# Performance work log

Hardware: AMD Instinct MI355X
Metric: run time of the kernel (lower is better)

## Reference

```python
import jax, jax.numpy as jnp
import numpy as np

N_NODES = 50000
N_EDGES = 800000
IN_CH, HID_CH, OUT_CH = 256, 128, 64


def setup_inputs() -> dict:
    key = jax.random.key(0)
    k_x, k_e, k_w1, k_w2 = jax.random.split(key, 4)
    x = jax.random.normal(k_x, (N_NODES, IN_CH), dtype=jnp.float32)
    edge_index = jax.random.randint(k_e, (2, N_EDGES), 0, N_NODES, dtype=jnp.int32)
    # Glorot-style init like PyG GCNConv (weight [in, out], bias zeros)
    s1 = float(np.sqrt(6.0 / (IN_CH + HID_CH)))
    s2 = float(np.sqrt(6.0 / (HID_CH + OUT_CH)))
    W1 = jax.random.uniform(k_w1, (IN_CH, HID_CH), jnp.float32, -s1, s1)
    b1 = jnp.zeros((HID_CH,), jnp.float32)
    W2 = jax.random.uniform(k_w2, (HID_CH, OUT_CH), jnp.float32, -s2, s2)
    b2 = jnp.zeros((OUT_CH,), jnp.float32)
    return {"x": x, "edge_index": edge_index, "W1": W1, "b1": b1, "W2": W2, "b2": b2}


def _gcn_conv(x, src, dst, deg_inv_sqrt, W, b, n_nodes):
    """GCNConv with self-loops: D^{-1/2}(A+I)D^{-1/2} X W + b."""
    h = x @ W  # [N, out]
    norm = deg_inv_sqrt[src] * deg_inv_sqrt[dst]          # [E]
    msgs = h[src] * norm[:, None]                          # [E, out] gather
    agg = jax.ops.segment_sum(msgs, dst, num_segments=n_nodes)  # scatter-add
    self_loop = h * (deg_inv_sqrt * deg_inv_sqrt)[:, None]      # self-loop term
    return agg + self_loop + b


def reference(x, edge_index, W1, b1, W2, b2):
    n = x.shape[0]
    src, dst = edge_index[0], edge_index[1]
    # degree includes self-loop (+1), edge weight 1, counted at destination
    deg = jnp.zeros((n,), x.dtype).at[dst].add(1.0) + 1.0
    dis = jax.lax.rsqrt(deg)
    h = jax.nn.relu(_gcn_conv(x, src, dst, dis, W1, b1, n))
    out = jax.nn.relu(_gcn_conv(h, src, dst, dis, W2, b2, n))
    return out
```

## Files before the change

kernel.cpp:

```cpp
#include <hip/hip_runtime.h>

#define N_NODES 50000
#define N_EDGES 800000
#define IN_CH 256
#define HID_CH 128
#define OUT_CH 64
#define CAP 64
#define NBINS 196
#define BINCAP 8192
#define PCHUNK 3200
#define PBLOCKS 250
#define SWZ_ELEMS (IN_CH * HID_CH + HID_CH * OUT_CH)
#define SWZ_BLOCKS (SWZ_ELEMS / 256)

typedef _Float16 f16;
typedef _Float16 f16x8 __attribute__((ext_vector_type(8)));
typedef float f32x4 __attribute__((ext_vector_type(4)));
typedef unsigned short u16;
typedef unsigned int u32;

template <int K, int N>
__device__ __forceinline__ void swz(const float* __restrict__ W, f16* __restrict__ Bsw,
                                    int idx) {
    constexpr int NTILES = N / 16;
    int j = idx & 7;
    int lane = (idx >> 3) & 63;
    int rest = idx >> 9;
    int nt = rest % NTILES;
    int ks = rest / NTILES;
    int k = ks * 32 + (lane >> 4) * 8 + j;
    int n = nt * 16 + (lane & 15);
    Bsw[idx] = (f16)W[(size_t)k * N + n];
}

__global__ __launch_bounds__(256) void k_place(const int* __restrict__ src,
                                               const int* __restrict__ dst,
                                               int* __restrict__ binCursor,
                                               u32* __restrict__ ebuf,
                                               const float* __restrict__ W1,
                                               const float* __restrict__ W2,
                                               f16* __restrict__ B1,
                                               f16* __restrict__ B2) {
    if ((int)blockIdx.x >= PBLOCKS) {
        int idx = ((int)blockIdx.x - PBLOCKS) * 256 + threadIdx.x;
        if (idx < IN_CH * HID_CH) {
            swz<IN_CH, HID_CH>(W1, B1, idx);
        } else {
            idx -= IN_CH * HID_CH;
            if (idx < HID_CH * OUT_CH) swz<HID_CH, OUT_CH>(W2, B2, idx);
        }
        return;
    }
    __shared__ u32 codes[PCHUNK];
    __shared__ int lcnt[NBINS], lbase[NBINS], lcur[NBINS];
    for (int i = threadIdx.x; i < NBINS; i += 256) lcnt[i] = 0;
    __syncthreads();
    int base = blockIdx.x * PCHUNK;
    for (int j = threadIdx.x; j < PCHUNK; j += 256) {
        u32 d = (u32)dst[base + j];
        codes[j] = (d << 16) | (u32)src[base + j];
        atomicAdd(&lcnt[d >> 8], 1);
    }
    __syncthreads();
    for (int i = threadIdx.x; i < NBINS; i += 256) {
        lbase[i] = i * BINCAP + atomicAdd(&binCursor[i], lcnt[i]);
        lcur[i] = 0;
    }
    __syncthreads();
    for (int j = threadIdx.x; j < PCHUNK; j += 256) {
        u32 c = codes[j];
        int b = c >> 24;
        int p = atomicAdd(&lcur[b], 1);
        int pos = lbase[b] + p;
        if (pos < (b + 1) * BINCAP) ebuf[pos] = c;
    }
}

__global__ __launch_bounds__(256) void k_build(const u32* __restrict__ ebuf,
                                               const int* __restrict__ binCursor,
                                               int* __restrict__ cnt,
                                               float* __restrict__ dis,
                                               u16* __restrict__ bucket, int N) {
    __shared__ int lcnt[256];
    __shared__ u16 lbuck[256 * CAP];
    int t = threadIdx.x;
    lcnt[t] = 0;
    __syncthreads();
    int b = blockIdx.x;
    int count = binCursor[b];
    if (count > BINCAP) count = BINCAP;
    int s = b * BINCAP;
    int e = s + count;
    for (int i = s + t; i < e; i += 256) {
        u32 c = ebuf[i];
        int local = (c >> 16) & 255;
        int p = atomicAdd(&lcnt[local], 1);
        if (p < CAP) lbuck[local * CAP + p] = (u16)(c & 0xFFFFu);
    }
    __syncthreads();
    int nodeBase = b << 8;
    if (nodeBase + t < N) {
        cnt[nodeBase + t] = lcnt[t];
        dis[nodeBase + t] = rsqrtf((float)lcnt[t] + 1.0f);
    }
    const uint4* lsrc = (const uint4*)lbuck;
    uint4* gdst = (uint4*)(bucket + (size_t)nodeBase * CAP);
    for (int idx = t; idx < 256 * CAP / 8; idx += 256) {
        int row = idx >> 3;
        int chunk = idx & 7;
        if (nodeBase + row < N && (chunk << 3) < lcnt[row]) gdst[idx] = lsrc[idx];
    }
}

__global__ __launch_bounds__(256) void k_gemm1(const float* __restrict__ A,
                                               const f16* __restrict__ Bsw,
                                               const float* __restrict__ dis,
                                               f16* __restrict__ C, int M) {
    constexpr int K = IN_CH, N = HID_CH;
    constexpr int KSTEPS = K / 32, NTILES = N / 16;
    const int tid = threadIdx.x;
    const int wave = tid >> 6, lane = tid & 63;
    const int quad = lane >> 4, l16 = lane & 15;
    int row = blockIdx.x * 64 + wave * 16 + l16;
    const int rowc = row < M ? row : M - 1;

    f32x4 acc[NTILES];
#pragma unroll
    for (int t = 0; t < NTILES; ++t) acc[t] = (f32x4){0.f, 0.f, 0.f, 0.f};

#pragma unroll
    for (int ks = 0; ks < KSTEPS; ++ks) {
        f16x8 afrag;
        const float4* p = (const float4*)(A + (size_t)rowc * K + ks * 32 + quad * 8);
        float4 v0 = p[0], v1 = p[1];
        afrag[0] = (f16)v0.x; afrag[1] = (f16)v0.y;
        afrag[2] = (f16)v0.z; afrag[3] = (f16)v0.w;
        afrag[4] = (f16)v1.x; afrag[5] = (f16)v1.y;
        afrag[6] = (f16)v1.z; afrag[7] = (f16)v1.w;
#pragma unroll
        for (int t = 0; t < NTILES; ++t) {
            f16x8 bfrag = *(const f16x8*)(Bsw + (((size_t)ks * NTILES + t) * 64 + lane) * 8);
            acc[t] = __builtin_amdgcn_mfma_f32_16x16x32_f16(afrag, bfrag, acc[t], 0, 0, 0);
        }
    }

    int rbase = blockIdx.x * 64 + wave * 16 + quad * 4;
#pragma unroll
    for (int r = 0; r < 4; ++r) {
        int gr = rbase + r;
        if (gr < M) {
            float d = dis[gr];
#pragma unroll
            for (int t = 0; t < NTILES; ++t)
                C[(size_t)gr * N + t * 16 + l16] = (f16)(acc[t][r] * d);
        }
    }
}

__global__ __launch_bounds__(256) void k_pullgemm(const f16* __restrict__ g1,
                                                  const float* __restrict__ dis,
                                                  const float* __restrict__ b1,
                                                  const int* __restrict__ cnt,
                                                  const u16* __restrict__ bucket,
                                                  const f16* __restrict__ B2sw,
                                                  f16* __restrict__ g2) {
    constexpr int LDSW = HID_CH + 8;
    __shared__ f16 aggl[64 * LDSW];
    const int tid = threadIdx.x;
    const int sub = tid & 15;
    const int nl = tid >> 4;
    const int blockBase = (int)blockIdx.x * 64;

    const float4* b1p = (const float4*)(b1 + sub * 8);
    float4 bb0 = b1p[0], bb1 = b1p[1];
    float bv[8] = {bb0.x, bb0.y, bb0.z, bb0.w, bb1.x, bb1.y, bb1.z, bb1.w};

    for (int it = 0; it < 4; ++it) {
        int lrow = it * 16 + nl;
        int u = blockBase + lrow;
        f16x8 o;
        if (u < N_NODES) {
            const f16* gp = g1 + sub * 8;
            f16x8 sv = *(const f16x8*)(gp + (size_t)u * HID_CH);
            float a[8];
#pragma unroll
            for (int j = 0; j < 8; ++j) a[j] = (float)sv[j];

            int n = cnt[u];
            if (n > CAP) n = CAP;
            const u16* row = bucket + u * CAP;

            int k = 0;
            for (; k + 8 <= n; k += 8) {
                uint4 iv = *(const uint4*)(row + k);
                int s0 = iv.x & 0xFFFF, s1 = iv.x >> 16;
                int s2 = iv.y & 0xFFFF, s3 = iv.y >> 16;
                int s4 = iv.z & 0xFFFF, s5 = iv.z >> 16;
                int s6 = iv.w & 0xFFFF, s7 = iv.w >> 16;
                f16x8 v0 = *(const f16x8*)(gp + (size_t)s0 * HID_CH);
                f16x8 v1 = *(const f16x8*)(gp + (size_t)s1 * HID_CH);
                f16x8 v2 = *(const f16x8*)(gp + (size_t)s2 * HID_CH);
                f16x8 v3 = *(const f16x8*)(gp + (size_t)s3 * HID_CH);
                f16x8 v4 = *(const f16x8*)(gp + (size_t)s4 * HID_CH);
                f16x8 v5 = *(const f16x8*)(gp + (size_t)s5 * HID_CH);
                f16x8 v6 = *(const f16x8*)(gp + (size_t)s6 * HID_CH);
                f16x8 v7 = *(const f16x8*)(gp + (size_t)s7 * HID_CH);
#pragma unroll
                for (int j = 0; j < 8; ++j)
                    a[j] += (((float)v0[j] + (float)v1[j]) + ((float)v2[j] + (float)v3[j])) +
                            (((float)v4[j] + (float)v5[j]) + ((float)v6[j] + (float)v7[j]));
            }
            if (k + 4 <= n) {
                ushort4 s4v = *(const ushort4*)(row + k);
                f16x8 v0 = *(const f16x8*)(gp + (size_t)s4v.x * HID_CH);
                f16x8 v1 = *(const f16x8*)(gp + (size_t)s4v.y * HID_CH);
                f16x8 v2 = *(const f16x8*)(gp + (size_t)s4v.z * HID_CH);
                f16x8 v3 = *(const f16x8*)(gp + (size_t)s4v.w * HID_CH);
#pragma unroll
                for (int j = 0; j < 8; ++j)
                    a[j] += ((float)v0[j] + (float)v1[j]) + ((float)v2[j] + (float)v3[j]);
                k += 4;
            }
            for (; k < n; ++k) {
                f16x8 v = *(const f16x8*)(gp + (size_t)row[k] * HID_CH);
#pragma unroll
                for (int j = 0; j < 8; ++j) a[j] += (float)v[j];
            }

            float du = dis[u];
#pragma unroll
            for (int j = 0; j < 8; ++j) {
                float t = fmaf(du, a[j], bv[j]);
                o[j] = (f16)(t > 0.f ? t : 0.f);
            }
        } else {
#pragma unroll
            for (int j = 0; j < 8; ++j) o[j] = (f16)0;
        }
        *(f16x8*)(aggl + (size_t)lrow * LDSW + sub * 8) = o;
    }
    __syncthreads();

    constexpr int KSTEPS = HID_CH / 32, NTILES = OUT_CH / 16;
    const int wave = tid >> 6, lane = tid & 63;
    const int quad = lane >> 4, l16 = lane & 15;
    const int lrowA = wave * 16 + l16;

    f32x4 acc[NTILES];
#pragma unroll
    for (int t = 0; t < NTILES; ++t) acc[t] = (f32x4){0.f, 0.f, 0.f, 0.f};

#pragma unroll
    for (int ks = 0; ks < KSTEPS; ++ks) {
        f16x8 afrag = *(const f16x8*)(aggl + (size_t)lrowA * LDSW + ks * 32 + quad * 8);
#pragma unroll
        for (int t = 0; t < NTILES; ++t) {
            f16x8 bfrag = *(const f16x8*)(B2sw + (((size_t)ks * NTILES + t) * 64 + lane) * 8);
            acc[t] = __builtin_amdgcn_mfma_f32_16x16x32_f16(afrag, bfrag, acc[t], 0, 0, 0);
        }
    }

    int rbase = blockBase + wave * 16 + quad * 4;
#pragma unroll
    for (int r = 0; r < 4; ++r) {
        int gr = rbase + r;
        if (gr < N_NODES) {
            float d = dis[gr];
#pragma unroll
            for (int t = 0; t < NTILES; ++t)
                g2[(size_t)gr * OUT_CH + t * 16 + l16] = (f16)(acc[t][r] * d);
        }
    }
}

__global__ __launch_bounds__(256) void k_pull2(const f16* __restrict__ g2,
                                               const float* __restrict__ dis,
                                               const float* __restrict__ b2,
                                               const int* __restrict__ cnt,
                                               const u16* __restrict__ bucket,
                                               float* __restrict__ out) {
    int gtid = blockIdx.x * 256 + threadIdx.x;
    int u = gtid >> 3;
    int sub = gtid & 7;
    if (u >= N_NODES) return;
    const f16* gp = g2 + sub * 8;

    f16x8 sv = *(const f16x8*)(gp + (size_t)u * OUT_CH);
    float a[8];
#pragma unroll
    for (int j = 0; j < 8; ++j) a[j] = (float)sv[j];

    int n = cnt[u];
    if (n > CAP) n = CAP;
    const u16* row = bucket + u * CAP;

    int k = 0;
    for (; k + 8 <= n; k += 8) {
        uint4 iv = *(const uint4*)(row + k);
        int s0 = iv.x & 0xFFFF, s1 = iv.x >> 16;
        int s2 = iv.y & 0xFFFF, s3 = iv.y >> 16;
        int s4 = iv.z & 0xFFFF, s5 = iv.z >> 16;
        int s6 = iv.w & 0xFFFF, s7 = iv.w >> 16;
        f16x8 v0 = *(const f16x8*)(gp + (size_t)s0 * OUT_CH);
        f16x8 v1 = *(const f16x8*)(gp + (size_t)s1 * OUT_CH);
        f16x8 v2 = *(const f16x8*)(gp + (size_t)s2 * OUT_CH);
        f16x8 v3 = *(const f16x8*)(gp + (size_t)s3 * OUT_CH);
        f16x8 v4 = *(const f16x8*)(gp + (size_t)s4 * OUT_CH);
        f16x8 v5 = *(const f16x8*)(gp + (size_t)s5 * OUT_CH);
        f16x8 v6 = *(const f16x8*)(gp + (size_t)s6 * OUT_CH);
        f16x8 v7 = *(const f16x8*)(gp + (size_t)s7 * OUT_CH);
#pragma unroll
        for (int j = 0; j < 8; ++j)
            a[j] += (((float)v0[j] + (float)v1[j]) + ((float)v2[j] + (float)v3[j])) +
                    (((float)v4[j] + (float)v5[j]) + ((float)v6[j] + (float)v7[j]));
    }
    if (k + 4 <= n) {
        ushort4 s4v = *(const ushort4*)(row + k);
        f16x8 v0 = *(const f16x8*)(gp + (size_t)s4v.x * OUT_CH);
        f16x8 v1 = *(const f16x8*)(gp + (size_t)s4v.y * OUT_CH);
        f16x8 v2 = *(const f16x8*)(gp + (size_t)s4v.z * OUT_CH);
        f16x8 v3 = *(const f16x8*)(gp + (size_t)s4v.w * OUT_CH);
#pragma unroll
        for (int j = 0; j < 8; ++j)
            a[j] += ((float)v0[j] + (float)v1[j]) + ((float)v2[j] + (float)v3[j]);
        k += 4;
    }
    for (; k < n; ++k) {
        f16x8 v = *(const f16x8*)(gp + (size_t)row[k] * OUT_CH);
#pragma unroll
        for (int j = 0; j < 8; ++j) a[j] += (float)v[j];
    }

    float du = dis[u];
    float4* op = (float4*)(out + (size_t)u * OUT_CH + sub * 8);
    float4 o0, o1;
    o0.x = fmaxf(fmaf(du, a[0], b2[sub * 8 + 0]), 0.f);
    o0.y = fmaxf(fmaf(du, a[1], b2[sub * 8 + 1]), 0.f);
    o0.z = fmaxf(fmaf(du, a[2], b2[sub * 8 + 2]), 0.f);
    o0.w = fmaxf(fmaf(du, a[3], b2[sub * 8 + 3]), 0.f);
    o1.x = fmaxf(fmaf(du, a[4], b2[sub * 8 + 4]), 0.f);
    o1.y = fmaxf(fmaf(du, a[5], b2[sub * 8 + 5]), 0.f);
    o1.z = fmaxf(fmaf(du, a[6], b2[sub * 8 + 6]), 0.f);
    o1.w = fmaxf(fmaf(du, a[7], b2[sub * 8 + 7]), 0.f);
    op[0] = o0;
    op[1] = o1;
}


extern "C" void kernel_launch(void* const* d_in, const int* in_sizes, int n_in,
                              void* d_out, int out_size, void* d_ws, size_t ws_size,
                              hipStream_t stream) {
    const float* x  = (const float*)d_in[0];
    const int* ei   = (const int*)d_in[1];
    const float* W1 = (const float*)d_in[2];
    const float* b1 = (const float*)d_in[3];
    const float* W2 = (const float*)d_in[4];
    const float* b2 = (const float*)d_in[5];
    float* out = (float*)d_out;

    const int* src = ei;
    const int* dst = ei + N_EDGES;

    char* ws = (char*)d_ws;
    size_t off = 0;
    auto alloc = [&](size_t bytes) -> void* {
        off = (off + 255) & ~(size_t)255;
        void* p = ws + off;
        off += bytes;
        return p;
    };
    int*   binCursor = (int*)alloc((size_t)NBINS * 4);
    u32*   ebuf      = (u32*)alloc((size_t)NBINS * BINCAP * 4);
    int*   cnt       = (int*)alloc((size_t)N_NODES * 4);
    float* dis       = (float*)alloc((size_t)N_NODES * 4);
    u16*   bucket    = (u16*)alloc((size_t)N_NODES * CAP * 2);
    f16*   W1sw      = (f16*)alloc((size_t)IN_CH * HID_CH * 2);
    f16*   W2sw      = (f16*)alloc((size_t)HID_CH * OUT_CH * 2);
    f16*   g1        = (f16*)alloc((size_t)N_NODES * HID_CH * 2);
    f16*   g2        = (f16*)alloc((size_t)N_NODES * OUT_CH * 2);

    hipMemsetAsync(binCursor, 0, (size_t)NBINS * 4, stream);

    k_place<<<PBLOCKS + SWZ_BLOCKS, 256, 0, stream>>>(src, dst, binCursor, ebuf,
                                                      W1, W2, W1sw, W2sw);
    k_build<<<NBINS, 256, 0, stream>>>(ebuf, binCursor, cnt, dis, bucket, N_NODES);

    k_gemm1<<<(N_NODES + 63) / 64, 256, 0, stream>>>(x, W1sw, dis, g1, N_NODES);

    k_pullgemm<<<(N_NODES + 63) / 64, 256, 0, stream>>>(g1, dis, b1, cnt, bucket,
                                                        W2sw, g2);

    k_pull2<<<(N_NODES * 8 + 255) / 256, 256, 0, stream>>>(g2, dis, b2, cnt, bucket, out);
}
```

Baseline: 186.6 us.

## Merge bucket build and first GEMM into one launch, move source scaling to pull

The CSR bucket build and the first dense GEMM now run as a single kernel: the first NBINS blocks build the buckets and the rest compute x@W1. Because the GEMM no longer waits for degrees, it writes unscaled h. The pull kernel applies the source-side dis[s] scaling per neighbour instead. This removes a launch and the serialization between the two independent stages. In exchange each gathered edge needs an extra random 4-byte dis load and a multiply, and the large smem footprint of the build path also limits occupancy for the GEMM blocks.

```diff
diff --git a/kernel.cpp b/kernel.cpp
--- a/kernel.cpp
+++ b/kernel.cpp
@@ -12,6 +12,7 @@
 #define PBLOCKS 250
 #define SWZ_ELEMS (IN_CH * HID_CH + HID_CH * OUT_CH)
 #define SWZ_BLOCKS (SWZ_ELEMS / 256)
+#define GEMM1_BLOCKS ((N_NODES + 63) / 64)
 
 typedef _Float16 f16;
 typedef _Float16 f16x8 __attribute__((ext_vector_type(8)));
@@ -76,57 +77,57 @@
     }
 }
 
-__global__ __launch_bounds__(256) void k_build(const u32* __restrict__ ebuf,
-                                               const int* __restrict__ binCursor,
-                                               int* __restrict__ cnt,
-                                               float* __restrict__ dis,
-                                               u16* __restrict__ bucket, int N) {
+__global__ __launch_bounds__(256) void k_buildmm(const u32* __restrict__ ebuf,
+                                                 const int* __restrict__ binCursor,
+                                                 int* __restrict__ cnt,
+                                                 float* __restrict__ dis,
+                                                 u16* __restrict__ bucket,
+                                                 const float* __restrict__ A,
+                                                 const f16* __restrict__ Bsw,
+                                                 f16* __restrict__ C) {
     __shared__ int lcnt[256];
     __shared__ u16 lbuck[256 * CAP];
     int t = threadIdx.x;
-    lcnt[t] = 0;
-    __syncthreads();
-    int b = blockIdx.x;
-    int count = binCursor[b];
-    if (count > BINCAP) count = BINCAP;
-    int s = b * BINCAP;
-    int e = s + count;
-    for (int i = s + t; i < e; i += 256) {
-        u32 c = ebuf[i];
-        int local = (c >> 16) & 255;
-        int p = atomicAdd(&lcnt[local], 1);
-        if (p < CAP) lbuck[local * CAP + p] = (u16)(c & 0xFFFFu);
-    }
-    __syncthreads();
-    int nodeBase = b << 8;
-    if (nodeBase + t < N) {
-        cnt[nodeBase + t] = lcnt[t];
-        dis[nodeBase + t] = rsqrtf((float)lcnt[t] + 1.0f);
-    }
-    const uint4* lsrc = (const uint4*)lbuck;
-    uint4* gdst = (uint4*)(bucket + (size_t)nodeBase * CAP);
-    for (int idx = t; idx < 256 * CAP / 8; idx += 256) {
-        int row = idx >> 3;
-        int chunk = idx & 7;
-        if (nodeBase + row < N && (chunk << 3) < lcnt[row]) gdst[idx] = lsrc[idx];
-    }
-}
-
-__global__ __launch_bounds__(256) void k_gemm1(const float* __restrict__ A,
-                                               const f16* __restrict__ Bsw,
-                                               const float* __restrict__ dis,
-                                               f16* __restrict__ C, int M) {
+    if ((int)blockIdx.x < NBINS) {
+        lcnt[t] = 0;
+        __syncthreads();
+        int b = blockIdx.x;
+        int count = binCursor[b];
+        if (count > BINCAP) count = BINCAP;
+        int s = b * BINCAP;
+        int e = s + count;
+        for (int i = s + t; i < e; i += 256) {
+            u32 c = ebuf[i];
+            int local = (c >> 16) & 255;
+            int p = atomicAdd(&lcnt[local], 1);
+            if (p < CAP) lbuck[local * CAP + p] = (u16)(c & 0xFFFFu);
+        }
+        __syncthreads();
+        int nodeBase = b << 8;
+        if (nodeBase + t < N_NODES) {
+            cnt[nodeBase + t] = lcnt[t];
+            dis[nodeBase + t] = rsqrtf((float)lcnt[t] + 1.0f);
+        }
+        const uint4* lsrc = (const uint4*)lbuck;
+        uint4* gdst = (uint4*)(bucket + (size_t)nodeBase * CAP);
+        for (int idx = t; idx < 256 * CAP / 8; idx += 256) {
+            int row = idx >> 3;
+            int chunk = idx & 7;
+            if (nodeBase + row < N_NODES && (chunk << 3) < lcnt[row]) gdst[idx] = lsrc[idx];
+        }
+        return;
+    }
     constexpr int K = IN_CH, N = HID_CH;
     constexpr int KSTEPS = K / 32, NTILES = N / 16;
-    const int tid = threadIdx.x;
-    const int wave = tid >> 6, lane = tid & 63;
+    const int mb = (int)blockIdx.x - NBINS;
+    const int wave = t >> 6, lane = t & 63;
     const int quad = lane >> 4, l16 = lane & 15;
-    int row = blockIdx.x * 64 + wave * 16 + l16;
-    const int rowc = row < M ? row : M - 1;
+    int row = mb * 64 + wave * 16 + l16;
+    const int rowc = row < N_NODES ? row : N_NODES - 1;
 
     f32x4 acc[NTILES];
 #pragma unroll
-    for (int t = 0; t < NTILES; ++t) acc[t] = (f32x4){0.f, 0.f, 0.f, 0.f};
+    for (int tt = 0; tt < NTILES; ++tt) acc[tt] = (f32x4){0.f, 0.f, 0.f, 0.f};
 
 #pragma unroll
     for (int ks = 0; ks < KSTEPS; ++ks) {
@@ -138,21 +139,20 @@
         afrag[4] = (f16)v1.x; afrag[5] = (f16)v1.y;
         afrag[6] = (f16)v1.z; afrag[7] = (f16)v1.w;
 #pragma unroll
-        for (int t = 0; t < NTILES; ++t) {
-            f16x8 bfrag = *(const f16x8*)(Bsw + (((size_t)ks * NTILES + t) * 64 + lane) * 8);
-            acc[t] = __builtin_amdgcn_mfma_f32_16x16x32_f16(afrag, bfrag, acc[t], 0, 0, 0);
-        }
-    }
-
-    int rbase = blockIdx.x * 64 + wave * 16 + quad * 4;
+        for (int tt = 0; tt < NTILES; ++tt) {
+            f16x8 bfrag = *(const f16x8*)(Bsw + (((size_t)ks * NTILES + tt) * 64 + lane) * 8);
+            acc[tt] = __builtin_amdgcn_mfma_f32_16x16x32_f16(afrag, bfrag, acc[tt], 0, 0, 0);
+        }
+    }
+
+    int rbase = mb * 64 + wave * 16 + quad * 4;
 #pragma unroll
     for (int r = 0; r < 4; ++r) {
         int gr = rbase + r;
-        if (gr < M) {
-            float d = dis[gr];
-#pragma unroll
-            for (int t = 0; t < NTILES; ++t)
-                C[(size_t)gr * N + t * 16 + l16] = (f16)(acc[t][r] * d);
+        if (gr < N_NODES) {
+#pragma unroll
+            for (int tt = 0; tt < NTILES; ++tt)
+                C[(size_t)gr * N + tt * 16 + l16] = (f16)acc[tt][r];
         }
     }
 }
@@ -180,11 +180,12 @@
         int u = blockBase + lrow;
         f16x8 o;
         if (u < N_NODES) {
+            float du = dis[u];
             const f16* gp = g1 + sub * 8;
             f16x8 sv = *(const f16x8*)(gp + (size_t)u * HID_CH);
             float a[8];
 #pragma unroll
-            for (int j = 0; j < 8; ++j) a[j] = (float)sv[j];
+            for (int j = 0; j < 8; ++j) a[j] = du * (float)sv[j];
 
             int n = cnt[u];
             if (n > CAP) n = CAP;
@@ -197,6 +198,8 @@
                 int s2 = iv.y & 0xFFFF, s3 = iv.y >> 16;
                 int s4 = iv.z & 0xFFFF, s5 = iv.z >> 16;
                 int s6 = iv.w & 0xFFFF, s7 = iv.w >> 16;
+                float d0 = dis[s0], d1 = dis[s1], d2 = dis[s2], d3 = dis[s3];
+                float d4 = dis[s4], d5 = dis[s5], d6 = dis[s6], d7 = dis[s7];
                 f16x8 v0 = *(const f16x8*)(gp + (size_t)s0 * HID_CH);
                 f16x8 v1 = *(const f16x8*)(gp + (size_t)s1 * HID_CH);
                 f16x8 v2 = *(const f16x8*)(gp + (size_t)s2 * HID_CH);
@@ -207,27 +210,32 @@
                 f16x8 v7 = *(const f16x8*)(gp + (size_t)s7 * HID_CH);
 #pragma unroll
                 for (int j = 0; j < 8; ++j)
-                    a[j] += (((float)v0[j] + (float)v1[j]) + ((float)v2[j] + (float)v3[j])) +
-                            (((float)v4[j] + (float)v5[j]) + ((float)v6[j] + (float)v7[j]));
+                    a[j] += ((d0 * (float)v0[j] + d1 * (float)v1[j]) +
+                             (d2 * (float)v2[j] + d3 * (float)v3[j])) +
+                            ((d4 * (float)v4[j] + d5 * (float)v5[j]) +
+                             (d6 * (float)v6[j] + d7 * (float)v7[j]));
             }
             if (k + 4 <= n) {
                 ushort4 s4v = *(const ushort4*)(row + k);
+                float d0 = dis[s4v.x], d1 = dis[s4v.y], d2 = dis[s4v.z], d3 = dis[s4v.w];
                 f16x8 v0 = *(const f16x8*)(gp + (size_t)s4v.x * HID_CH);
                 f16x8 v1 = *(const f16x8*)(gp + (size_t)s4v.y * HID_CH);
                 f16x8 v2 = *(const f16x8*)(gp + (size_t)s4v.z * HID_CH);
                 f16x8 v3 = *(const f16x8*)(gp + (size_t)s4v.w * HID_CH);
 #pragma unroll
                 for (int j = 0; j < 8; ++j)
-                    a[j] += ((float)v0[j] + (float)v1[j]) + ((float)v2[j] + (float)v3[j]);
+                    a[j] += (d0 * (float)v0[j] + d1 * (float)v1[j]) +
+                            (d2 * (float)v2[j] + d3 * (float)v3[j]);
                 k += 4;
             }
             for (; k < n; ++k) {
-                f16x8 v = *(const f16x8*)(gp + (size_t)row[k] * HID_CH);
-#pragma unroll
-                for (int j = 0; j < 8; ++j) a[j] += (float)v[j];
+                int s = row[k];
+                float ds = dis[s];
+                f16x8 v = *(const f16x8*)(gp + (size_t)s * HID_CH);
+#pragma unroll
+                for (int j = 0; j < 8; ++j) a[j] += ds * (float)v[j];
             }
 
-            float du = dis[u];
 #pragma unroll
             for (int j = 0; j < 8; ++j) {
                 float t = fmaf(du, a[j], bv[j]);
@@ -383,9 +391,8 @@
 
     k_place<<<PBLOCKS + SWZ_BLOCKS, 256, 0, stream>>>(src, dst, binCursor, ebuf,
                                                       W1, W2, W1sw, W2sw);
-    k_build<<<NBINS, 256, 0, stream>>>(ebuf, binCursor, cnt, dis, bucket, N_NODES);
-
-    k_gemm1<<<(N_NODES + 63) / 64, 256, 0, stream>>>(x, W1sw, dis, g1, N_NODES);
+    k_buildmm<<<NBINS + GEMM1_BLOCKS, 256, 0, stream>>>(ebuf, binCursor, cnt, dis,
+                                                        bucket, x, W1sw, g1);
 
     k_pullgemm<<<(N_NODES + 63) / 64, 256, 0, stream>>>(g1, dis, b1, cnt, bucket,
                                                         W2sw, g2);
```

After: 195.0 us. +4.5%, slower.

## Store feature matrices in 32-column panels to shrink gather working set

Applied to the files above, without the earlier changes.

The g1 and g2 intermediates are now written in column-panel-major order: each 32-wide slice of channels is stored contiguously for all nodes. The pull kernels run one panel at a time, with 4 threads per node, so the working set gathered in each pass is a quarter (or half) of the full feature matrix. This aims to improve L2/MALL hit rates for the random neighbor gathers. The trade-off is that the neighbor index list is re-read once per panel, each gather fetches only 64 bytes, and there is less parallelism per node.

```diff
diff --git a/kernel.cpp b/kernel.cpp
--- a/kernel.cpp
+++ b/kernel.cpp
@@ -152,7 +152,8 @@
             float d = dis[gr];
 #pragma unroll
             for (int t = 0; t < NTILES; ++t)
-                C[(size_t)gr * N + t * 16 + l16] = (f16)(acc[t][r] * d);
+                C[((size_t)(t >> 1) * N_NODES + gr) * 32 + (t & 1) * 16 + l16] =
+                    (f16)(acc[t][r] * d);
         }
     }
 }
@@ -167,28 +168,30 @@
     constexpr int LDSW = HID_CH + 8;
     __shared__ f16 aggl[64 * LDSW];
     const int tid = threadIdx.x;
-    const int sub = tid & 15;
-    const int nl = tid >> 4;
+    const int sub4 = tid & 3;
+    const int nl = tid >> 2;
     const int blockBase = (int)blockIdx.x * 64;
-
-    const float4* b1p = (const float4*)(b1 + sub * 8);
-    float4 bb0 = b1p[0], bb1 = b1p[1];
-    float bv[8] = {bb0.x, bb0.y, bb0.z, bb0.w, bb1.x, bb1.y, bb1.z, bb1.w};
-
-    for (int it = 0; it < 4; ++it) {
-        int lrow = it * 16 + nl;
-        int u = blockBase + lrow;
+    const int u = blockBase + nl;
+    const bool live = (u < N_NODES);
+
+    float du = 0.f;
+    int n = 0;
+    const u16* row = bucket;
+    if (live) {
+        du = dis[u];
+        n = cnt[u];
+        if (n > CAP) n = CAP;
+        row = bucket + (size_t)u * CAP;
+    }
+
+    for (int p = 0; p < 4; ++p) {
         f16x8 o;
-        if (u < N_NODES) {
-            const f16* gp = g1 + sub * 8;
-            f16x8 sv = *(const f16x8*)(gp + (size_t)u * HID_CH);
+        if (live) {
+            const f16* gp = g1 + ((size_t)p * N_NODES) * 32 + sub4 * 8;
+            f16x8 sv = *(const f16x8*)(gp + (size_t)u * 32);
             float a[8];
 #pragma unroll
             for (int j = 0; j < 8; ++j) a[j] = (float)sv[j];
-
-            int n = cnt[u];
-            if (n > CAP) n = CAP;
-            const u16* row = bucket + u * CAP;
 
             int k = 0;
             for (; k + 8 <= n; k += 8) {
@@ -197,14 +200,14 @@
                 int s2 = iv.y & 0xFFFF, s3 = iv.y >> 16;
                 int s4 = iv.z & 0xFFFF, s5 = iv.z >> 16;
                 int s6 = iv.w & 0xFFFF, s7 = iv.w >> 16;
-                f16x8 v0 = *(const f16x8*)(gp + (size_t)s0 * HID_CH);
-                f16x8 v1 = *(const f16x8*)(gp + (size_t)s1 * HID_CH);
-                f16x8 v2 = *(const f16x8*)(gp + (size_t)s2 * HID_CH);
-                f16x8 v3 = *(const f16x8*)(gp + (size_t)s3 * HID_CH);
-                f16x8 v4 = *(const f16x8*)(gp + (size_t)s4 * HID_CH);
-                f16x8 v5 = *(const f16x8*)(gp + (size_t)s5 * HID_CH);
-                f16x8 v6 = *(const f16x8*)(gp + (size_t)s6 * HID_CH);
-                f16x8 v7 = *(const f16x8*)(gp + (size_t)s7 * HID_CH);
+                f16x8 v0 = *(const f16x8*)(gp + (size_t)s0 * 32);
+                f16x8 v1 = *(const f16x8*)(gp + (size_t)s1 * 32);
+                f16x8 v2 = *(const f16x8*)(gp + (size_t)s2 * 32);
+                f16x8 v3 = *(const f16x8*)(gp + (size_t)s3 * 32);
+                f16x8 v4 = *(const f16x8*)(gp + (size_t)s4 * 32);
+                f16x8 v5 = *(const f16x8*)(gp + (size_t)s5 * 32);
+                f16x8 v6 = *(const f16x8*)(gp + (size_t)s6 * 32);
+                f16x8 v7 = *(const f16x8*)(gp + (size_t)s7 * 32);
 #pragma unroll
                 for (int j = 0; j < 8; ++j)
                     a[j] += (((float)v0[j] + (float)v1[j]) + ((float)v2[j] + (float)v3[j])) +
@@ -212,22 +215,24 @@
             }
             if (k + 4 <= n) {
                 ushort4 s4v = *(const ushort4*)(row + k);
-                f16x8 v0 = *(const f16x8*)(gp + (size_t)s4v.x * HID_CH);
-                f16x8 v1 = *(const f16x8*)(gp + (size_t)s4v.y * HID_CH);
-                f16x8 v2 = *(const f16x8*)(gp + (size_t)s4v.z * HID_CH);
-                f16x8 v3 = *(const f16x8*)(gp + (size_t)s4v.w * HID_CH);
+                f16x8 v0 = *(const f16x8*)(gp + (size_t)s4v.x * 32);
+                f16x8 v1 = *(const f16x8*)(gp + (size_t)s4v.y * 32);
+                f16x8 v2 = *(const f16x8*)(gp + (size_t)s4v.z * 32);
+                f16x8 v3 = *(const f16x8*)(gp + (size_t)s4v.w * 32);
 #pragma unroll
                 for (int j = 0; j < 8; ++j)
                     a[j] += ((float)v0[j] + (float)v1[j]) + ((float)v2[j] + (float)v3[j]);
                 k += 4;
             }
             for (; k < n; ++k) {
-                f16x8 v = *(const f16x8*)(gp + (size_t)row[k] * HID_CH);
+                f16x8 v = *(const f16x8*)(gp + (size_t)row[k] * 32);
 #pragma unroll
                 for (int j = 0; j < 8; ++j) a[j] += (float)v[j];
             }
 
-            float du = dis[u];
+            const float4* bp = (const float4*)(b1 + p * 32 + sub4 * 8);
+            float4 B0 = bp[0], B1v = bp[1];
+            float bv[8] = {B0.x, B0.y, B0.z, B0.w, B1v.x, B1v.y, B1v.z, B1v.w};
 #pragma unroll
             for (int j = 0; j < 8; ++j) {
                 float t = fmaf(du, a[j], bv[j]);
@@ -237,7 +242,7 @@
 #pragma unroll
             for (int j = 0; j < 8; ++j) o[j] = (f16)0;
         }
-        *(f16x8*)(aggl + (size_t)lrow * LDSW + sub * 8) = o;
+        *(f16x8*)(aggl + (size_t)nl * LDSW + p * 32 + sub4 * 8) = o;
     }
     __syncthreads();
 
@@ -268,7 +273,8 @@
             float d = dis[gr];
 #pragma unroll
             for (int t = 0; t < NTILES; ++t)
-                g2[(size_t)gr * OUT_CH + t * 16 + l16] = (f16)(acc[t][r] * d);
+                g2[((size_t)(t >> 1) * N_NODES + gr) * 32 + (t & 1) * 16 + l16] =
+                    (f16)(acc[t][r] * d);
         }
     }
 }
@@ -279,71 +285,75 @@
                                                const int* __restrict__ cnt,
                                                const u16* __restrict__ bucket,
                                                float* __restrict__ out) {
-    int gtid = blockIdx.x * 256 + threadIdx.x;
-    int u = gtid >> 3;
-    int sub = gtid & 7;
+    const int tid = threadIdx.x;
+    const int sub4 = tid & 3;
+    const int nl = tid >> 2;
+    const int u = (int)blockIdx.x * 64 + nl;
     if (u >= N_NODES) return;
-    const f16* gp = g2 + sub * 8;
-
-    f16x8 sv = *(const f16x8*)(gp + (size_t)u * OUT_CH);
-    float a[8];
-#pragma unroll
-    for (int j = 0; j < 8; ++j) a[j] = (float)sv[j];
-
+
+    float du = dis[u];
     int n = cnt[u];
     if (n > CAP) n = CAP;
-    const u16* row = bucket + u * CAP;
-
-    int k = 0;
-    for (; k + 8 <= n; k += 8) {
-        uint4 iv = *(const uint4*)(row + k);
-        int s0 = iv.x & 0xFFFF, s1 = iv.x >> 16;
-        int s2 = iv.y & 0xFFFF, s3 = iv.y >> 16;
-        int s4 = iv.z & 0xFFFF, s5 = iv.z >> 16;
-        int s6 = iv.w & 0xFFFF, s7 = iv.w >> 16;
-        f16x8 v0 = *(const f16x8*)(gp + (size_t)s0 * OUT_CH);
-        f16x8 v1 = *(const f16x8*)(gp + (size_t)s1 * OUT_CH);
-        f16x8 v2 = *(const f16x8*)(gp + (size_t)s2 * OUT_CH);
-        f16x8 v3 = *(const f16x8*)(gp + (size_t)s3 * OUT_CH);
-        f16x8 v4 = *(const f16x8*)(gp + (size_t)s4 * OUT_CH);
-        f16x8 v5 = *(const f16x8*)(gp + (size_t)s5 * OUT_CH);
-        f16x8 v6 = *(const f16x8*)(gp + (size_t)s6 * OUT_CH);
-        f16x8 v7 = *(const f16x8*)(gp + (size_t)s7 * OUT_CH);
-#pragma unroll
-        for (int j = 0; j < 8; ++j)
-            a[j] += (((float)v0[j] + (float)v1[j]) + ((float)v2[j] + (float)v3[j])) +
-                    (((float)v4[j] + (float)v5[j]) + ((float)v6[j] + (float)v7[j]));
-    }
-    if (k + 4 <= n) {
-        ushort4 s4v = *(const ushort4*)(row + k);
-        f16x8 v0 = *(const f16x8*)(gp + (size_t)s4v.x * OUT_CH);
-        f16x8 v1 = *(const f16x8*)(gp + (size_t)s4v.y * OUT_CH);
-        f16x8 v2 = *(const f16x8*)(gp + (size_t)s4v.z * OUT_CH);
-        f16x8 v3 = *(const f16x8*)(gp + (size_t)s4v.w * OUT_CH);
-#pragma unroll
-        for (int j = 0; j < 8; ++j)
-            a[j] += ((float)v0[j] + (float)v1[j]) + ((float)v2[j] + (float)v3[j]);
-        k += 4;
-    }
-    for (; k < n; ++k) {
-        f16x8 v = *(const f16x8*)(gp + (size_t)row[k] * OUT_CH);
-#pragma unroll
-        for (int j = 0; j < 8; ++j) a[j] += (float)v[j];
-    }
-
-    float du = dis[u];
-    float4* op = (float4*)(out + (size_t)u * OUT_CH + sub * 8);
-    float4 o0, o1;
-    o0.x = fmaxf(fmaf(du, a[0], b2[sub * 8 + 0]), 0.f);
-    o0.y = fmaxf(fmaf(du, a[1], b2[sub * 8 + 1]), 0.f);
-    o0.z = fmaxf(fmaf(du, a[2], b2[sub * 8 + 2]), 0.f);
-    o0.w = fmaxf(fmaf(du, a[3], b2[sub * 8 + 3]), 0.f);
-    o1.x = fmaxf(fmaf(du, a[4], b2[sub * 8 + 4]), 0.f);
-    o1.y = fmaxf(fmaf(du, a[5], b2[sub * 8 + 5]), 0.f);
-    o1.z = fmaxf(fmaf(du, a[6], b2[sub * 8 + 6]), 0.f);
-    o1.w = fmaxf(fmaf(du, a[7], b2[sub * 8 + 7]), 0.f);
-    op[0] = o0;
-    op[1] = o1;
+    const u16* row = bucket + (size_t)u * CAP;
+
+    for (int p = 0; p < 2; ++p) {
+        const f16* gp = g2 + ((size_t)p * N_NODES) * 32 + sub4 * 8;
+        f16x8 sv = *(const f16x8*)(gp + (size_t)u * 32);
+        float a[8];
+#pragma unroll
+        for (int j = 0; j < 8; ++j) a[j] = (float)sv[j];
+
+        int k = 0;
+        for (; k + 8 <= n; k += 8) {
+            uint4 iv = *(const uint4*)(row + k);
+            int s0 = iv.x & 0xFFFF, s1 = iv.x >> 16;
+            int s2 = iv.y & 0xFFFF, s3 = iv.y >> 16;
+            int s4 = iv.z & 0xFFFF, s5 = iv.z >> 16;
+            int s6 = iv.w & 0xFFFF, s7 = iv.w >> 16;
+            f16x8 v0 = *(const f16x8*)(gp + (size_t)s0 * 32);
+            f16x8 v1 = *(const f16x8*)(gp + (size_t)s1 * 32);
+            f16x8 v2 = *(const f16x8*)(gp + (size_t)s2 * 32);
+            f16x8 v3 = *(const f16x8*)(gp + (size_t)s3 * 32);
+            f16x8 v4 = *(const f16x8*)(gp + (size_t)s4 * 32);
+            f16x8 v5 = *(const f16x8*)(gp + (size_t)s5 * 32);
+            f16x8 v6 = *(const f16x8*)(gp + (size_t)s6 * 32);
+            f16x8 v7 = *(const f16x8*)(gp + (size_t)s7 * 32);
+#pragma unroll
+            for (int j = 0; j < 8; ++j)
+                a[j] += (((float)v0[j] + (float)v1[j]) + ((float)v2[j] + (float)v3[j])) +
+                        (((float)v4[j] + (float)v5[j]) + ((float)v6[j] + (float)v7[j]));
+        }
+        if (k + 4 <= n) {
+            ushort4 s4v = *(const ushort4*)(row + k);
+            f16x8 v0 = *(const f16x8*)(gp + (size_t)s4v.x * 32);
+            f16x8 v1 = *(const f16x8*)(gp + (size_t)s4v.y * 32);
+            f16x8 v2 = *(const f16x8*)(gp + (size_t)s4v.z * 32);
+            f16x8 v3 = *(const f16x8*)(gp + (size_t)s4v.w * 32);
+#pragma unroll
+            for (int j = 0; j < 8; ++j)
+                a[j] += ((float)v0[j] + (float)v1[j]) + ((float)v2[j] + (float)v3[j]);
+            k += 4;
+        }
+        for (; k < n; ++k) {
+            f16x8 v = *(const f16x8*)(gp + (size_t)row[k] * 32);
+#pragma unroll
+            for (int j = 0; j < 8; ++j) a[j] += (float)v[j];
+        }
+
+        const float* bp = b2 + p * 32 + sub4 * 8;
+        float4* op = (float4*)(out + (size_t)u * OUT_CH + p * 32 + sub4 * 8);
+        float4 o0, o1;
+        o0.x = fmaxf(fmaf(du, a[0], bp[0]), 0.f);
+        o0.y = fmaxf(fmaf(du, a[1], bp[1]), 0.f);
+        o0.z = fmaxf(fmaf(du, a[2], bp[2]), 0.f);
+        o0.w = fmaxf(fmaf(du, a[3], bp[3]), 0.f);
+        o1.x = fmaxf(fmaf(du, a[4], bp[4]), 0.f);
+        o1.y = fmaxf(fmaf(du, a[5], bp[5]), 0.f);
+        o1.z = fmaxf(fmaf(du, a[6], bp[6]), 0.f);
+        o1.w = fmaxf(fmaf(du, a[7], bp[7]), 0.f);
+        op[0] = o0;
+        op[1] = o1;
+    }
 }
 
 
@@ -390,5 +400,5 @@
     k_pullgemm<<<(N_NODES + 63) / 64, 256, 0, stream>>>(g1, dis, b1, cnt, bucket,
                                                         W2sw, g2);
 
-    k_pull2<<<(N_NODES * 8 + 255) / 256, 256, 0, stream>>>(g2, dis, b2, cnt, bucket, out);
-}
+    k_pull2<<<(N_NODES + 63) / 64, 256, 0, stream>>>(g2, dis, b2, cnt, bucket, out);
+}
```

After: 193.7 us. 1.04x slower.
